# Performance work log

Hardware: AMD Instinct MI355X
Metric: run time of the kernel (lower is better)

The kernel has to match this reference:

```python
import jax, jax.numpy as jnp
import numpy as np

B, T, CIN, H = 64, 256, 512, 1024


def setup_inputs() -> dict:
    key = jax.random.key(0)
    ks = jax.random.split(key, 9)
    s_in = 1.0 / np.sqrt(H)
    return {
        "x": jax.random.normal(ks[0], (B, T, CIN), dtype=jnp.float32),
        "Wih0": jax.random.normal(ks[1], (4 * H, CIN), dtype=jnp.float32) * s_in,
        "Whh0": jax.random.normal(ks[2], (4 * H, H), dtype=jnp.float32) * s_in,
        "bih0": jax.random.normal(ks[3], (4 * H,), dtype=jnp.float32) * s_in,
        "bhh0": jax.random.normal(ks[4], (4 * H,), dtype=jnp.float32) * s_in,
        "Wih1": jax.random.normal(ks[5], (4 * H, H), dtype=jnp.float32) * s_in,
        "Whh1": jax.random.normal(ks[6], (4 * H, H), dtype=jnp.float32) * s_in,
        "bih1": jax.random.normal(ks[7], (4 * H,), dtype=jnp.float32) * s_in,
        "bhh1": jax.random.normal(ks[8], (4 * H,), dtype=jnp.float32) * s_in,
    }


def _lstm_cell(xt, h, c, Wih, Whh, bih, bhh):
    # PyTorch LSTMCell gate order: i, f, g, o
    gates = xt @ Wih.T + h @ Whh.T + bih + bhh  # [B, 4H]
    i, f, g, o = jnp.split(gates, 4, axis=-1)
    i = jax.nn.sigmoid(i)
    f = jax.nn.sigmoid(f)
    g = jnp.tanh(g)
    o = jax.nn.sigmoid(o)
    c_new = f * c + i * g
    h_new = o * jnp.tanh(c_new)
    return h_new, c_new


def reference(x, Wih0, Whh0, bih0, bhh0, Wih1, Whh1, bih1, bhh1):
    b = x.shape[0]
    zeros = jnp.zeros((b, H), dtype=x.dtype)
    init = (zeros, zeros, zeros, zeros)  # h0, c0, h1, c1 (zeros init)

    def step(carry, xt):
        h0, c0, h1, c1 = carry
        h0, c0 = _lstm_cell(xt, h0, c0, Wih0, Whh0, bih0, bhh0)
        h1, c1 = _lstm_cell(h0, h1, c1, Wih1, Whh1, bih1, bhh1)
        return (h0, c0, h1, c1), None

    (h0, c0, h1, c1), _ = jax.lax.scan(step, init, jnp.swapaxes(x, 0, 1))
    # module stacks per-step outputs then returns only the last timestep
    return h1
```

## Files before the change

### kernel.cpp

```cpp
#include <hip/hip_runtime.h>
#include <stdint.h>

#define BB   64
#define TT   256
#define CIN  512
#define HH   1024
#define NBLK 192
#define NTHR 256

#define OFF_WP0 0ull
#define OFF_WP1 12582912ull
#define OFF_XP  29360128ull
#define OFF_B0S 46137344ull
#define OFF_B1S 46153728ull
#define OFF_H0  46170112ull
#define OFF_H1  46694400ull
#define OFF_FLG 47218688ull
#define SZ_HP   131072ull
#define ZERO_SZ (8*SZ_HP + 1024)

typedef short bf16x8 __attribute__((ext_vector_type(8)));
typedef float f32x4 __attribute__((ext_vector_type(4)));
typedef int   i32x4 __attribute__((ext_vector_type(4)));

__device__ i32x4 llvm_amdgcn_raw_buffer_load_i32x4(i32x4 srsrc, int voffset, int soffset,
                                                   int cachepolicy) __asm("llvm.amdgcn.raw.buffer.load.v4i32");
__device__ void  llvm_amdgcn_raw_buffer_store_i32x4(i32x4 vdata, i32x4 srsrc, int voffset,
                                                    int soffset, int cachepolicy) __asm("llvm.amdgcn.raw.buffer.store.v4i32");
#define CP_SC01 17

static __device__ __forceinline__ i32x4 make_srd(const char* p) {
  i32x4 r;
  r.x = (int)(uint32_t)(uintptr_t)p;
  r.y = (int)(uint32_t)((uintptr_t)p >> 32);
  r.z = (int)0xFFFFFFFF;
  r.w = 0x00020000;
  return r;
}
static __device__ __forceinline__ uint4 bload(i32x4 srd, int voff) {
  return __builtin_bit_cast(uint4, llvm_amdgcn_raw_buffer_load_i32x4(srd, voff, 0, CP_SC01));
}
static __device__ __forceinline__ void bstore(i32x4 srd, int voff, uint4 v) {
  llvm_amdgcn_raw_buffer_store_i32x4(__builtin_bit_cast(i32x4, v), srd, voff, 0, CP_SC01);
}

static __device__ __forceinline__ uint16_t f2b(float f) {
  union { float f; uint32_t u; } v; v.f = f;
  uint32_t r = (v.u + 0x7FFFu + ((v.u >> 16) & 1u)) >> 16;
  return (uint16_t)r;
}
static __device__ __forceinline__ uint4 cvt8(const float* s) {
  uint4 o;
  o.x = (uint32_t)f2b(s[0]) | ((uint32_t)f2b(s[1]) << 16);
  o.y = (uint32_t)f2b(s[2]) | ((uint32_t)f2b(s[3]) << 16);
  o.z = (uint32_t)f2b(s[4]) | ((uint32_t)f2b(s[5]) << 16);
  o.w = (uint32_t)f2b(s[6]) | ((uint32_t)f2b(s[7]) << 16);
  return o;
}
static __device__ __forceinline__ f32x4 mfma16(uint4 a, uint4 b, f32x4 c) {
  return __builtin_amdgcn_mfma_f32_16x16x32_bf16(
      __builtin_bit_cast(bf16x8, a), __builtin_bit_cast(bf16x8, b), c, 0, 0, 0);
}
static __device__ __forceinline__ float sigm(float x)  { return 1.0f / (1.0f + __expf(-x)); }
static __device__ __forceinline__ float tanhx(float x) { return 1.0f - 2.0f / (__expf(2.0f * x) + 1.0f); }

__global__ void pack_w0(const float* __restrict__ wih, const float* __restrict__ whh,
                        char* __restrict__ ws) {
  uint32_t u = blockIdx.x * blockDim.x + threadIdx.x;
  int lane = u & 63;
  uint32_t idx = u >> 6;
  int j = (int)(idx % 48u);
  uint32_t r2 = idx / 48u;
  int w = r2 & 3, bw = r2 >> 2;
  int c = (j & 3) * 16 + (lane & 15);
  int g_row = (c & 3) * 1024 + bw * 16 + (c >> 2);
  uint4 v;
  if (j < 16) {
    int k = w * 128 + (j >> 2) * 32 + (lane >> 4) * 8;
    v = cvt8(wih + (size_t)g_row * 512 + k);
  } else {
    int k = w * 256 + ((j - 16) >> 2) * 32 + (lane >> 4) * 8;
    v = cvt8(whh + (size_t)g_row * 1024 + k);
  }
  ((uint4*)(ws + OFF_WP0))[u] = v;
}
__global__ void pack_w1(const float* __restrict__ wih, const float* __restrict__ whh,
                        char* __restrict__ ws) {
  uint32_t u = blockIdx.x * blockDim.x + threadIdx.x;
  int lane = u & 63;
  int j = (u >> 6) & 31;
  int w = (u >> 11) & 3;
  int bw = u >> 13;
  int c = (j & 1) * 16 + (lane & 15);
  int g_row = (c & 3) * 1024 + bw * 8 + (c >> 2);
  int k = w * 512 + (j >> 1) * 32 + (lane >> 4) * 8;
  uint4 v;
  if (k < 1024) v = cvt8(wih + (size_t)g_row * 1024 + k);
  else          v = cvt8(whh + (size_t)g_row * 1024 + (k - 1024));
  ((uint4*)(ws + OFF_WP1))[u] = v;
}
__global__ void pack_x(const float* __restrict__ x, char* __restrict__ ws) {
  uint32_t u = blockIdx.x * blockDim.x + threadIdx.x;
  int lane = u & 63;
  int F = (u >> 6) & 63;
  int t = u >> 12;
  int r = (F & 3) * 16 + (lane & 15);
  int k = (F >> 2) * 32 + (lane >> 4) * 8;
  ((uint4*)(ws + OFF_XP))[u] = cvt8(x + (size_t)r * (TT * CIN) + (size_t)t * CIN + k);
}
__global__ void pack_bias(const float* __restrict__ bih0, const float* __restrict__ bhh0,
                          const float* __restrict__ bih1, const float* __restrict__ bhh1,
                          char* __restrict__ ws) {
  uint32_t v = blockIdx.x * blockDim.x + threadIdx.x;
  if (v < 4096) ((float*)(ws + OFF_B0S))[v] = bih0[v] + bhh0[v];
  else          ((float*)(ws + OFF_B1S))[v - 4096] = bih1[v - 4096] + bhh1[v - 4096];
}

static __device__ __forceinline__ void wait_L0(uint32_t* fl, int tgt) {
  const int lane = threadIdx.x & 63;
  for (;;) {
    int f0 = (int)__hip_atomic_load(fl + lane,       __ATOMIC_RELAXED, __HIP_MEMORY_SCOPE_AGENT);
    int f1 = (int)__hip_atomic_load(fl + 64 + lane,  __ATOMIC_RELAXED, __HIP_MEMORY_SCOPE_AGENT);
    int f2 = (int)__hip_atomic_load(fl + 128 + lane, __ATOMIC_RELAXED, __HIP_MEMORY_SCOPE_AGENT);
    int mn1 = f1 < f2 ? f1 : f2;
    if (__all(f0 >= tgt && mn1 >= tgt - 2)) break;
    __builtin_amdgcn_s_sleep(1);
  }
  __builtin_amdgcn_fence(__ATOMIC_ACQUIRE, "workgroup");
}
static __device__ __forceinline__ void wait_L1a(uint32_t* fl, int tgt) {
  const int lane = threadIdx.x & 63;
  for (;;) {
    int f0 = (int)__hip_atomic_load(fl + lane, __ATOMIC_RELAXED, __HIP_MEMORY_SCOPE_AGENT);
    if (__all(f0 >= tgt)) break;
    __builtin_amdgcn_s_sleep(1);
  }
  __builtin_amdgcn_fence(__ATOMIC_ACQUIRE, "workgroup");
}
static __device__ __forceinline__ void wait_L1b(uint32_t* fl, int tgt) {
  const int lane = threadIdx.x & 63;
  for (;;) {
    int f1 = (int)__hip_atomic_load(fl + 64 + lane,  __ATOMIC_RELAXED, __HIP_MEMORY_SCOPE_AGENT);
    int f2 = (int)__hip_atomic_load(fl + 128 + lane, __ATOMIC_RELAXED, __HIP_MEMORY_SCOPE_AGENT);
    int mn = f1 < f2 ? f1 : f2;
    if (__all(mn >= tgt)) break;
    __builtin_amdgcn_s_sleep(1);
  }
  __builtin_amdgcn_fence(__ATOMIC_ACQUIRE, "workgroup");
}

__global__ __launch_bounds__(NTHR, 1) void lstm_persist(char* __restrict__ ws,
                                                        float* __restrict__ out) {
  __shared__ float cpart[16384];
  __shared__ __align__(16) uint16_t hreg[1024];
  const int tid = threadIdx.x, blk = blockIdx.x;
  const int wave = tid >> 6, lane = tid & 63;
  const bool isL1 = blk >= 64;
  const int bw = isL1 ? blk - 64 : blk;
  uint32_t* flags = (uint32_t*)(ws + OFF_FLG);

  const int eu  = isL1 ? (tid & 7)  : (tid & 15);
  const int erb = isL1 ? (tid >> 3) : (tid >> 4);
  const int ug  = isL1 ? (bw * 8 + eu) : (bw * 16 + eu);
  const float* bsrc = (const float*)(ws + (isL1 ? OFF_B1S : OFF_B0S));
  const float bs0 = bsrc[ug], bs1 = bsrc[1024 + ug], bs2 = bsrc[2048 + ug], bs3 = bsrc[3072 + ug];
  float cst[4] = {0.f, 0.f, 0.f, 0.f};

  uint4 b[48];
  if (isL1) {
    const uint4* bp = (const uint4*)(ws + OFF_WP1) + ((size_t)(bw * 4 + wave) * 32) * 64 + lane;
    #pragma unroll
    for (int j = 0; j < 32; ++j) b[j] = bp[(size_t)j * 64];
  } else {
    const uint4* bp = (const uint4*)(ws + OFF_WP0) + ((size_t)(bw * 4 + wave) * 48) * 64 + lane;
    #pragma unroll
    for (int j = 0; j < 48; ++j) b[j] = bp[(size_t)j * 64];
  }

  for (int p = 0; p <= 256; ++p) {
    f32x4 acc[4][4];
    #pragma unroll
    for (int rf = 0; rf < 4; ++rf)
      #pragma unroll
      for (int cf = 0; cf < 4; ++cf)
        acc[rf][cf] = (f32x4){0.f, 0.f, 0.f, 0.f};

    if (!isL1) {
      if (p == 256) break;
      const uint4* xpl = (const uint4*)(ws + OFF_XP) + (size_t)p * 4096 + lane;
      #pragma unroll
      for (int jx = 0; jx < 4; ++jx) {
        const int kf = wave * 4 + jx;
        uint4 a0 = xpl[kf * 256], a1 = xpl[kf * 256 + 64],
              a2 = xpl[kf * 256 + 128], a3 = xpl[kf * 256 + 192];
        #pragma unroll
        for (int cf = 0; cf < 4; ++cf) {
          uint4 bb = b[jx * 4 + cf];
          acc[0][cf] = mfma16(a0, bb, acc[0][cf]);
          acc[1][cf] = mfma16(a1, bb, acc[1][cf]);
          acc[2][cf] = mfma16(a2, bb, acc[2][cf]);
          acc[3][cf] = mfma16(a3, bb, acc[3][cf]);
        }
      }
      if (p > 0) wait_L0(flags, p);
      const i32x4 srdh = make_srd(ws + OFF_H0 + (size_t)((p + 3) & 3) * SZ_HP);
      #pragma unroll
      for (int jh = 0; jh < 8; ++jh) {
        const int kf = wave * 8 + jh;
        const int base = (kf * 256 + lane) * 16;
        uint4 a0 = bload(srdh, base);
        uint4 a1 = bload(srdh, base + 64 * 16);
        uint4 a2 = bload(srdh, base + 128 * 16);
        uint4 a3 = bload(srdh, base + 192 * 16);
        #pragma unroll
        for (int cf = 0; cf < 4; ++cf) {
          uint4 bb = b[16 + jh * 4 + cf];
          acc[0][cf] = mfma16(a0, bb, acc[0][cf]);
          acc[1][cf] = mfma16(a1, bb, acc[1][cf]);
          acc[2][cf] = mfma16(a2, bb, acc[2][cf]);
          acc[3][cf] = mfma16(a3, bb, acc[3][cf]);
        }
      }
    } else {
      if (p == 0) {
        if (tid == 0)
          __hip_atomic_store(flags + blk, 1u, __ATOMIC_RELAXED, __HIP_MEMORY_SCOPE_AGENT);
        continue;
      }
      if (wave < 2) wait_L1a(flags, p);
      else          wait_L1b(flags, p);
      uint32_t boff = (uint32_t)(wave < 2 ? OFF_H0 : OFF_H1) + ((p + 3) & 3) * (uint32_t)SZ_HP;
      boff = __builtin_amdgcn_readfirstlane(boff);
      const i32x4 srdh = make_srd(ws + boff);
      const int kb = (wave & 1) * 16;
      #pragma unroll
      for (int jh = 0; jh < 16; ++jh) {
        const int kf = kb + jh;
        const int base = (kf * 256 + lane) * 16;
        uint4 a0 = bload(srdh, base);
        uint4 a1 = bload(srdh, base + 64 * 16);
        uint4 a2 = bload(srdh, base + 128 * 16);
        uint4 a3 = bload(srdh, base + 192 * 16);
        #pragma unroll
        for (int cf = 0; cf < 2; ++cf) {
          uint4 bb = b[jh * 2 + cf];
          acc[0][cf] = mfma16(a0, bb, acc[0][cf]);
          acc[1][cf] = mfma16(a1, bb, acc[1][cf]);
          acc[2][cf] = mfma16(a2, bb, acc[2][cf]);
          acc[3][cf] = mfma16(a3, bb, acc[3][cf]);
        }
      }
    }

    if (isL1) {
      #pragma unroll
      for (int rf = 0; rf < 4; ++rf)
        #pragma unroll
        for (int cf = 0; cf < 2; ++cf)
          *(f32x4*)&cpart[(((wave * 4 + rf) * 2 + cf) * 64 + lane) * 4] = acc[rf][cf];
    } else {
      #pragma unroll
      for (int rf = 0; rf < 4; ++rf)
        #pragma unroll
        for (int cf = 0; cf < 4; ++cf)
          *(f32x4*)&cpart[(((wave * 4 + rf) * 4 + cf) * 64 + lane) * 4] = acc[rf][cf];
    }
    __syncthreads();

    if (isL1) {
      #pragma unroll
      for (int half = 0; half < 2; ++half) {
        const int r64 = erb + half * 32;
        const int rf = r64 >> 4, r16 = r64 & 15;
        const int reg = r16 & 3, lbase = 16 * (r16 >> 2);
        float gs[4];
        #pragma unroll
        for (int g = 0; g < 4; ++g) {
          const int c = eu * 4 + g;
          const int lc = (c & 15) + lbase;
          const int cf = c >> 4;
          float s = 0.f;
          #pragma unroll
          for (int w = 0; w < 4; ++w)
            s += cpart[(((w * 4 + rf) * 2 + cf) * 64 + lc) * 4 + reg];
          gs[g] = s;
        }
        const float iv = sigm(gs[0] + bs0), fv = sigm(gs[1] + bs1);
        const float gv = tanhx(gs[2] + bs2), ov = sigm(gs[3] + bs3);
        float cs = cst[half];
        cs = fv * cs + iv * gv;
        cst[half] = cs;
        const float hv = ov * tanhx(cs);
        hreg[r64 * 8 + eu] = f2b(hv);
        if (p == 256) out[(size_t)r64 * 1024 + ug] = hv;
      }
    } else {
      #pragma unroll
      for (int half = 0; half < 4; ++half) {
        const int r64 = erb + half * 16;
        const int rf = half, r16 = erb;
        const int reg = r16 & 3, lbase = 16 * (r16 >> 2);
        float gs[4];
        #pragma unroll
        for (int g = 0; g < 4; ++g) {
          const int c = eu * 4 + g;
          const int lc = (c & 15) + lbase;
          const int cf = c >> 4;
          float s = 0.f;
          #pragma unroll
          for (int w = 0; w < 4; ++w)
            s += cpart[(((w * 4 + rf) * 4 + cf) * 64 + lc) * 4 + reg];
          gs[g] = s;
        }
        const float iv = sigm(gs[0] + bs0), fv = sigm(gs[1] + bs1);
        const float gv = tanhx(gs[2] + bs2), ov = sigm(gs[3] + bs3);
        float cs = cst[half];
        cs = fv * cs + iv * gv;
        cst[half] = cs;
        const float hv = ov * tanhx(cs);
        hreg[r64 * 16 + eu] = f2b(hv);
      }
    }
    __syncthreads();

    if (p < 256) {
      if (isL1) {
        if (tid < 64) {
          uint4 v = ((const uint4*)hreg)[tid];
          const i32x4 srdw = make_srd(ws + OFF_H1 + (size_t)(p & 3) * SZ_HP);
          const int off = ((bw >> 2) * 4 + (tid >> 4)) * 1024 + (bw & 3) * 256 + (tid & 15) * 16;
          bstore(srdw, off, v);
        }
      } else {
        if (tid < 128) {
          uint4 v = ((const uint4*)hreg)[tid];
          const i32x4 srdw = make_srd(ws + OFF_H0 + (size_t)(p & 3) * SZ_HP);
          const int off = ((bw >> 1) * 4 + (tid >> 5)) * 1024
                        + (2 * (bw & 1) + (tid & 1)) * 256 + ((tid >> 1) & 15) * 16;
          bstore(srdw, off, v);
        }
      }
      __syncthreads();
      if (tid == 0)
        __hip_atomic_store(flags + blk, (uint32_t)(p + 1), __ATOMIC_RELAXED, __HIP_MEMORY_SCOPE_AGENT);
    }
  }
}

extern "C" void kernel_launch(void* const* d_in, const int* in_sizes, int n_in,
                              void* d_out, int out_size, void* d_ws, size_t ws_size,
                              hipStream_t stream) {
  const float* x    = (const float*)d_in[0];
  const float* Wih0 = (const float*)d_in[1];
  const float* Whh0 = (const float*)d_in[2];
  const float* bih0 = (const float*)d_in[3];
  const float* bhh0 = (const float*)d_in[4];
  const float* Wih1 = (const float*)d_in[5];
  const float* Whh1 = (const float*)d_in[6];
  const float* bih1 = (const float*)d_in[7];
  const float* bhh1 = (const float*)d_in[8];
  char* ws = (char*)d_ws;
  float* out = (float*)d_out;

  hipMemsetAsync(ws + OFF_H0, 0, ZERO_SZ, stream);

  pack_w0  <<<3072, 256, 0, stream>>>(Wih0, Whh0, ws);
  pack_w1  <<<4096, 256, 0, stream>>>(Wih1, Whh1, ws);
  pack_x   <<<4096, 256, 0, stream>>>(x, ws);
  pack_bias<<<32,   256, 0, stream>>>(bih0, bhh0, bih1, bhh1, ws);

  void* args[] = {(void*)&ws, (void*)&out};
  hipError_t e = hipLaunchCooperativeKernel((const void*)lstm_persist, dim3(NBLK),
                                            dim3(NTHR), args, 0, stream);
  if (e != hipSuccess) {
    (void)hipGetLastError();
    lstm_persist<<<dim3(NBLK), dim3(NTHR), 0, stream>>>(ws, out);
  }
}
```

Before: 1.990 ms.

## Narrow per-wave flag waits, stream x-weights from memory, drop trailing barrier

Each wave now waits only on the producer blocks whose h slice it reads, plus a looser lag check on the others, instead of waiting on all relevant flags. This shortens the critical-path dependency in the recurrent pipeline. The layer-0 input-projection weights are read from global memory each step rather than held in 16 extra registers, which cuts register pressure. The h store and flag publish are done by wave 0 alone with an s_waitcnt instead of a block barrier. The risk is extra global traffic for the x weights and subtler memory-ordering correctness.

```diff
diff --git a/kernel.cpp b/kernel.cpp
--- a/kernel.cpp
+++ b/kernel.cpp
@@ -63,6 +63,9 @@
 }
 static __device__ __forceinline__ float sigm(float x)  { return 1.0f / (1.0f + __expf(-x)); }
 static __device__ __forceinline__ float tanhx(float x) { return 1.0f - 2.0f / (__expf(2.0f * x) + 1.0f); }
+static __device__ __forceinline__ int imin2(int a, int b) { return a < b ? a : b; }
+
+#define FLD(i) ((int)__hip_atomic_load(fl + (i), __ATOMIC_RELAXED, __HIP_MEMORY_SCOPE_AGENT))
 
 __global__ void pack_w0(const float* __restrict__ wih, const float* __restrict__ whh,
                         char* __restrict__ ws) {
@@ -116,34 +119,41 @@
   else          ((float*)(ws + OFF_B1S))[v - 4096] = bih1[v - 4096] + bhh1[v - 4096];
 }
 
-static __device__ __forceinline__ void wait_L0(uint32_t* fl, int tgt) {
+static __device__ __forceinline__ void wait_L0w(uint32_t* fl, int tgt, int wave) {
   const int lane = threadIdx.x & 63;
+  const int si = 16 * wave + (lane & 15);
   for (;;) {
-    int f0 = (int)__hip_atomic_load(fl + lane,       __ATOMIC_RELAXED, __HIP_MEMORY_SCOPE_AGENT);
-    int f1 = (int)__hip_atomic_load(fl + 64 + lane,  __ATOMIC_RELAXED, __HIP_MEMORY_SCOPE_AGENT);
-    int f2 = (int)__hip_atomic_load(fl + 128 + lane, __ATOMIC_RELAXED, __HIP_MEMORY_SCOPE_AGENT);
-    int mn1 = f1 < f2 ? f1 : f2;
-    if (__all(f0 >= tgt && mn1 >= tgt - 2)) break;
+    int fs = FLD(si);
+    int f0 = FLD(lane);
+    int f1 = FLD(64 + lane);
+    int f2 = FLD(128 + lane);
+    int mn = imin2(f0, imin2(f1, f2));
+    if (__all(fs >= tgt && mn >= tgt - 2)) break;
     __builtin_amdgcn_s_sleep(1);
   }
   __builtin_amdgcn_fence(__ATOMIC_ACQUIRE, "workgroup");
 }
-static __device__ __forceinline__ void wait_L1a(uint32_t* fl, int tgt) {
+static __device__ __forceinline__ void wait_L1a(uint32_t* fl, int tgt, int wave) {
   const int lane = threadIdx.x & 63;
+  const int si = 32 * wave + (lane & 31);
   for (;;) {
-    int f0 = (int)__hip_atomic_load(fl + lane, __ATOMIC_RELAXED, __HIP_MEMORY_SCOPE_AGENT);
-    if (__all(f0 >= tgt)) break;
+    int fs = FLD(si);
+    int f1 = FLD(64 + lane);
+    int f2 = FLD(128 + lane);
+    int mn = imin2(f1, f2);
+    if (__all(fs >= tgt && mn >= tgt - 2)) break;
     __builtin_amdgcn_s_sleep(1);
   }
   __builtin_amdgcn_fence(__ATOMIC_ACQUIRE, "workgroup");
 }
-static __device__ __forceinline__ void wait_L1b(uint32_t* fl, int tgt) {
+static __device__ __forceinline__ void wait_L1b(uint32_t* fl, int tgt, int wave) {
   const int lane = threadIdx.x & 63;
+  const int tb = (wave == 2) ? 64 : 128;
+  const int ob = (wave == 2) ? 128 : 64;
   for (;;) {
-    int f1 = (int)__hip_atomic_load(fl + 64 + lane,  __ATOMIC_RELAXED, __HIP_MEMORY_SCOPE_AGENT);
-    int f2 = (int)__hip_atomic_load(fl + 128 + lane, __ATOMIC_RELAXED, __HIP_MEMORY_SCOPE_AGENT);
-    int mn = f1 < f2 ? f1 : f2;
-    if (__all(mn >= tgt)) break;
+    int fs = FLD(tb + lane);
+    int fo = FLD(ob + lane);
+    if (__all(fs >= tgt && fo >= tgt - 2)) break;
     __builtin_amdgcn_s_sleep(1);
   }
   __builtin_amdgcn_fence(__ATOMIC_ACQUIRE, "workgroup");
@@ -166,15 +176,17 @@
   const float bs0 = bsrc[ug], bs1 = bsrc[1024 + ug], bs2 = bsrc[2048 + ug], bs3 = bsrc[3072 + ug];
   float cst[4] = {0.f, 0.f, 0.f, 0.f};
 
-  uint4 b[48];
+  uint4 b[32];
+  const uint4* bxs = nullptr;
   if (isL1) {
     const uint4* bp = (const uint4*)(ws + OFF_WP1) + ((size_t)(bw * 4 + wave) * 32) * 64 + lane;
     #pragma unroll
     for (int j = 0; j < 32; ++j) b[j] = bp[(size_t)j * 64];
   } else {
     const uint4* bp = (const uint4*)(ws + OFF_WP0) + ((size_t)(bw * 4 + wave) * 48) * 64 + lane;
+    bxs = bp;
     #pragma unroll
-    for (int j = 0; j < 48; ++j) b[j] = bp[(size_t)j * 64];
+    for (int j = 0; j < 32; ++j) b[j] = bp[(size_t)(16 + j) * 64];
   }
 
   for (int p = 0; p <= 256; ++p) {
@@ -195,14 +207,14 @@
               a2 = xpl[kf * 256 + 128], a3 = xpl[kf * 256 + 192];
         #pragma unroll
         for (int cf = 0; cf < 4; ++cf) {
-          uint4 bb = b[jx * 4 + cf];
+          uint4 bb = bxs[(size_t)(jx * 4 + cf) * 64];
           acc[0][cf] = mfma16(a0, bb, acc[0][cf]);
           acc[1][cf] = mfma16(a1, bb, acc[1][cf]);
           acc[2][cf] = mfma16(a2, bb, acc[2][cf]);
           acc[3][cf] = mfma16(a3, bb, acc[3][cf]);
         }
       }
-      if (p > 0) wait_L0(flags, p);
+      if (p > 0) wait_L0w(flags, p, wave);
       const i32x4 srdh = make_srd(ws + OFF_H0 + (size_t)((p + 3) & 3) * SZ_HP);
       #pragma unroll
       for (int jh = 0; jh < 8; ++jh) {
@@ -214,7 +226,7 @@
         uint4 a3 = bload(srdh, base + 192 * 16);
         #pragma unroll
         for (int cf = 0; cf < 4; ++cf) {
-          uint4 bb = b[16 + jh * 4 + cf];
+          uint4 bb = b[jh * 4 + cf];
           acc[0][cf] = mfma16(a0, bb, acc[0][cf]);
           acc[1][cf] = mfma16(a1, bb, acc[1][cf]);
           acc[2][cf] = mfma16(a2, bb, acc[2][cf]);
@@ -227,8 +239,8 @@
           __hip_atomic_store(flags + blk, 1u, __ATOMIC_RELAXED, __HIP_MEMORY_SCOPE_AGENT);
         continue;
       }
-      if (wave < 2) wait_L1a(flags, p);
-      else          wait_L1b(flags, p);
+      if (wave < 2) wait_L1a(flags, p, wave);
+      else          wait_L1b(flags, p, wave);
       uint32_t boff = (uint32_t)(wave < 2 ? OFF_H0 : OFF_H1) + ((p + 3) & 3) * (uint32_t)SZ_HP;
       boff = __builtin_amdgcn_readfirstlane(boff);
       const i32x4 srdh = make_srd(ws + boff);
@@ -323,25 +335,25 @@
     }
     __syncthreads();
 
-    if (p < 256) {
+    if (p < 256 && wave == 0) {
       if (isL1) {
-        if (tid < 64) {
-          uint4 v = ((const uint4*)hreg)[tid];
-          const i32x4 srdw = make_srd(ws + OFF_H1 + (size_t)(p & 3) * SZ_HP);
-          const int off = ((bw >> 2) * 4 + (tid >> 4)) * 1024 + (bw & 3) * 256 + (tid & 15) * 16;
+        uint4 v = ((const uint4*)hreg)[lane];
+        const i32x4 srdw = make_srd(ws + OFF_H1 + (size_t)(p & 3) * SZ_HP);
+        const int off = ((bw >> 2) * 4 + (lane >> 4)) * 1024 + (bw & 3) * 256 + (lane & 15) * 16;
+        bstore(srdw, off, v);
+      } else {
+        const i32x4 srdw = make_srd(ws + OFF_H0 + (size_t)(p & 3) * SZ_HP);
+        #pragma unroll
+        for (int h = 0; h < 2; ++h) {
+          const int t = lane + 64 * h;
+          uint4 v = ((const uint4*)hreg)[t];
+          const int off = ((bw >> 1) * 4 + (t >> 5)) * 1024
+                        + (2 * (bw & 1) + (t & 1)) * 256 + ((t >> 1) & 15) * 16;
           bstore(srdw, off, v);
         }
-      } else {
-        if (tid < 128) {
-          uint4 v = ((const uint4*)hreg)[tid];
-          const i32x4 srdw = make_srd(ws + OFF_H0 + (size_t)(p & 3) * SZ_HP);
-          const int off = ((bw >> 1) * 4 + (tid >> 5)) * 1024
-                        + (2 * (bw & 1) + (tid & 1)) * 256 + ((tid >> 1) & 15) * 16;
-          bstore(srdw, off, v);
-        }
-      }
-      __syncthreads();
-      if (tid == 0)
+      }
+      asm volatile("s_waitcnt vmcnt(0)" ::: "memory");
+      if (lane == 0)
         __hip_atomic_store(flags + blk, (uint32_t)(p + 1), __ATOMIC_RELAXED, __HIP_MEMORY_SCOPE_AGENT);
     }
   }
```

After: 2.648 ms. 1.33x slower.

## Stream input-projection weights from memory and pad LDS partial-sum rows

Applied to the files above, without the earlier changes.

Layer-0 blocks no longer keep the 16 input-weight fragments in registers. They reload them from global memory each step, which cuts the register array from 48 to 32 uint4 entries and lowers register pressure. The LDS partial-sum buffer is padded to a 65-entry row stride, meant to reduce bank conflicts during the cross-wave reduction. The trade is extra global or L2 traffic on every layer-0 step, although that work comes before the recurrent wait and may be hidden.

```diff
diff --git a/kernel.cpp b/kernel.cpp
--- a/kernel.cpp
+++ b/kernel.cpp
@@ -63,6 +63,10 @@
 }
 static __device__ __forceinline__ float sigm(float x)  { return 1.0f / (1.0f + __expf(-x)); }
 static __device__ __forceinline__ float tanhx(float x) { return 1.0f - 2.0f / (__expf(2.0f * x) + 1.0f); }
+static __device__ __forceinline__ int imin2(int a, int b) { return a < b ? a : b; }
+
+#define FLD(i) ((int)__hip_atomic_load(fl + (i), __ATOMIC_RELAXED, __HIP_MEMORY_SCOPE_AGENT))
+#define CROW 65
 
 __global__ void pack_w0(const float* __restrict__ wih, const float* __restrict__ whh,
                         char* __restrict__ ws) {
@@ -119,10 +123,10 @@
 static __device__ __forceinline__ void wait_L0(uint32_t* fl, int tgt) {
   const int lane = threadIdx.x & 63;
   for (;;) {
-    int f0 = (int)__hip_atomic_load(fl + lane,       __ATOMIC_RELAXED, __HIP_MEMORY_SCOPE_AGENT);
-    int f1 = (int)__hip_atomic_load(fl + 64 + lane,  __ATOMIC_RELAXED, __HIP_MEMORY_SCOPE_AGENT);
-    int f2 = (int)__hip_atomic_load(fl + 128 + lane, __ATOMIC_RELAXED, __HIP_MEMORY_SCOPE_AGENT);
-    int mn1 = f1 < f2 ? f1 : f2;
+    int f0 = FLD(lane);
+    int f1 = FLD(64 + lane);
+    int f2 = FLD(128 + lane);
+    int mn1 = imin2(f1, f2);
     if (__all(f0 >= tgt && mn1 >= tgt - 2)) break;
     __builtin_amdgcn_s_sleep(1);
   }
@@ -131,7 +135,7 @@
 static __device__ __forceinline__ void wait_L1a(uint32_t* fl, int tgt) {
   const int lane = threadIdx.x & 63;
   for (;;) {
-    int f0 = (int)__hip_atomic_load(fl + lane, __ATOMIC_RELAXED, __HIP_MEMORY_SCOPE_AGENT);
+    int f0 = FLD(lane);
     if (__all(f0 >= tgt)) break;
     __builtin_amdgcn_s_sleep(1);
   }
@@ -140,9 +144,9 @@
 static __device__ __forceinline__ void wait_L1b(uint32_t* fl, int tgt) {
   const int lane = threadIdx.x & 63;
   for (;;) {
-    int f1 = (int)__hip_atomic_load(fl + 64 + lane,  __ATOMIC_RELAXED, __HIP_MEMORY_SCOPE_AGENT);
-    int f2 = (int)__hip_atomic_load(fl + 128 + lane, __ATOMIC_RELAXED, __HIP_MEMORY_SCOPE_AGENT);
-    int mn = f1 < f2 ? f1 : f2;
+    int f1 = FLD(64 + lane);
+    int f2 = FLD(128 + lane);
+    int mn = imin2(f1, f2);
     if (__all(mn >= tgt)) break;
     __builtin_amdgcn_s_sleep(1);
   }
@@ -151,7 +155,7 @@
 
 __global__ __launch_bounds__(NTHR, 1) void lstm_persist(char* __restrict__ ws,
                                                         float* __restrict__ out) {
-  __shared__ float cpart[16384];
+  __shared__ float cpart[64 * CROW * 4];
   __shared__ __align__(16) uint16_t hreg[1024];
   const int tid = threadIdx.x, blk = blockIdx.x;
   const int wave = tid >> 6, lane = tid & 63;
@@ -166,15 +170,17 @@
   const float bs0 = bsrc[ug], bs1 = bsrc[1024 + ug], bs2 = bsrc[2048 + ug], bs3 = bsrc[3072 + ug];
   float cst[4] = {0.f, 0.f, 0.f, 0.f};
 
-  uint4 b[48];
+  uint4 b[32];
+  const uint4* bxs = nullptr;
   if (isL1) {
     const uint4* bp = (const uint4*)(ws + OFF_WP1) + ((size_t)(bw * 4 + wave) * 32) * 64 + lane;
     #pragma unroll
     for (int j = 0; j < 32; ++j) b[j] = bp[(size_t)j * 64];
   } else {
     const uint4* bp = (const uint4*)(ws + OFF_WP0) + ((size_t)(bw * 4 + wave) * 48) * 64 + lane;
+    bxs = bp;
     #pragma unroll
-    for (int j = 0; j < 48; ++j) b[j] = bp[(size_t)j * 64];
+    for (int j = 0; j < 32; ++j) b[j] = bp[(size_t)(16 + j) * 64];
   }
 
   for (int p = 0; p <= 256; ++p) {
@@ -195,7 +201,7 @@
               a2 = xpl[kf * 256 + 128], a3 = xpl[kf * 256 + 192];
         #pragma unroll
         for (int cf = 0; cf < 4; ++cf) {
-          uint4 bb = b[jx * 4 + cf];
+          uint4 bb = bxs[(size_t)(jx * 4 + cf) * 64];
           acc[0][cf] = mfma16(a0, bb, acc[0][cf]);
           acc[1][cf] = mfma16(a1, bb, acc[1][cf]);
           acc[2][cf] = mfma16(a2, bb, acc[2][cf]);
@@ -214,7 +220,7 @@
         uint4 a3 = bload(srdh, base + 192 * 16);
         #pragma unroll
         for (int cf = 0; cf < 4; ++cf) {
-          uint4 bb = b[16 + jh * 4 + cf];
+          uint4 bb = b[jh * 4 + cf];
           acc[0][cf] = mfma16(a0, bb, acc[0][cf]);
           acc[1][cf] = mfma16(a1, bb, acc[1][cf]);
           acc[2][cf] = mfma16(a2, bb, acc[2][cf]);
@@ -257,13 +263,13 @@
       for (int rf = 0; rf < 4; ++rf)
         #pragma unroll
         for (int cf = 0; cf < 2; ++cf)
-          *(f32x4*)&cpart[(((wave * 4 + rf) * 2 + cf) * 64 + lane) * 4] = acc[rf][cf];
+          *(f32x4*)&cpart[(((wave * 4 + rf) * 2 + cf) * CROW + lane) * 4] = acc[rf][cf];
     } else {
       #pragma unroll
       for (int rf = 0; rf < 4; ++rf)
         #pragma unroll
         for (int cf = 0; cf < 4; ++cf)
-          *(f32x4*)&cpart[(((wave * 4 + rf) * 4 + cf) * 64 + lane) * 4] = acc[rf][cf];
+          *(f32x4*)&cpart[(((wave * 4 + rf) * 4 + cf) * CROW + lane) * 4] = acc[rf][cf];
     }
     __syncthreads();
 
@@ -282,7 +288,7 @@
           float s = 0.f;
           #pragma unroll
           for (int w = 0; w < 4; ++w)
-            s += cpart[(((w * 4 + rf) * 2 + cf) * 64 + lc) * 4 + reg];
+            s += cpart[(((w * 4 + rf) * 2 + cf) * CROW + lc) * 4 + reg];
           gs[g] = s;
         }
         const float iv = sigm(gs[0] + bs0), fv = sigm(gs[1] + bs1);
@@ -309,7 +315,7 @@
           float s = 0.f;
           #pragma unroll
           for (int w = 0; w < 4; ++w)
-            s += cpart[(((w * 4 + rf) * 4 + cf) * 64 + lc) * 4 + reg];
+            s += cpart[(((w * 4 + rf) * 4 + cf) * CROW + lc) * 4 + reg];
           gs[g] = s;
         }
         const float iv = sigm(gs[0] + bs0), fv = sigm(gs[1] + bs1);
```

Measured after the change: 2.286 ms. 14.8% more time.
